# Kernel optimization log

Measured on AMD Instinct MI355X. Metric: run time of the kernel, lower is better.

Reference implementation:

```python
import jax, jax.numpy as jnp
import numpy as np
import math

B, L, D, H = 2, 2048, 1024, 16
HD = D // H          # head_dim = 64
DF = 4096            # d_feedforward
SIGMA = 0.02


def setup_inputs() -> dict:
    key = jax.random.key(0)
    ks = jax.random.split(key, 18)
    g = lambda k, shape: (jax.random.normal(k, shape, jnp.float32) * SIGMA)
    inp = {
        "x": jax.random.normal(ks[0], (B, L, D), jnp.float32),
        # causal mask: True above diagonal -> masked
        "causal_mask": jnp.triu(jnp.ones((L, L), dtype=bool), 1),
        # attention weights, stored [in, out] (math-equivalent to torch Linear)
        "Wq": g(ks[1], (D, D)), "bq": jnp.zeros((D,), jnp.float32),
        "Wk": g(ks[2], (D, D)), "bk": jnp.zeros((D,), jnp.float32),
        "Wv": g(ks[3], (D, D)), "bv": jnp.zeros((D,), jnp.float32),
        "Wo": g(ks[4], (D, D)), "bo": jnp.zeros((D,), jnp.float32),
        "ln1_g": jnp.ones((D,), jnp.float32), "ln1_b": jnp.zeros((D,), jnp.float32),
        "W1": g(ks[5], (D, DF)), "b1": jnp.zeros((DF,), jnp.float32),
        "W2": g(ks[6], (DF, D)), "b2": jnp.zeros((D,), jnp.float32),
        "ln2_g": jnp.ones((D,), jnp.float32), "ln2_b": jnp.zeros((D,), jnp.float32),
    }
    return inp


def _layernorm(x, g, b, eps=1e-5):
    m = jnp.mean(x, axis=-1, keepdims=True)
    v = jnp.mean((x - m) ** 2, axis=-1, keepdims=True)
    return (x - m) * jax.lax.rsqrt(v + eps) * g + b


def _rita_gelu(h):
    return h * 0.5 * (1.0 + jnp.tanh(0.79788456 * h * (1.0 + 0.044715 * h * h)))


def _rotate_half(x):
    x1, x2 = x[..., : x.shape[-1] // 2], x[..., x.shape[-1] // 2 :]
    return jnp.concatenate((-x2, x1), axis=-1)


def _rope_tables(seq_len, head_dim, dtype):
    inv_freq = 1.0 / (10000.0 ** (jnp.arange(0, head_dim, 2, dtype=jnp.float32) / head_dim))
    t = jnp.arange(seq_len, dtype=jnp.float32)
    freqs = jnp.einsum("i,j->ij", t, inv_freq)          # [L, HD/2]
    emb = jnp.concatenate((freqs, freqs), axis=-1)        # [L, HD]
    return jnp.cos(emb).astype(dtype)[None, None], jnp.sin(emb).astype(dtype)[None, None]


def reference(x, causal_mask, Wq, bq, Wk, bk, Wv, bv, Wo, bo,
              ln1_g, ln1_b, W1, b1, W2, b2, ln2_g, ln2_b):
    N, Lx, Dx = x.shape
    # --- attention block ---
    y = _layernorm(x, ln1_g, ln1_b)
    def heads(t):  # [N,L,D] -> [N,H,L,HD]
        return t.reshape(N, Lx, H, HD).transpose(0, 2, 1, 3)
    q = heads(y @ Wq + bq)
    k = heads(y @ Wk + bk)
    v = heads(y @ Wv + bv)
    cos, sin = _rope_tables(Lx, HD, x.dtype)
    q = q * cos + _rotate_half(q) * sin
    k = k * cos + _rotate_half(k) * sin
    att = jnp.einsum("nhqd,nhkd->nhqk", q, k) * (1.0 / math.sqrt(HD))
    att = jnp.where(causal_mask[None, None], jnp.float32(-jnp.inf).astype(att.dtype), att)
    att = jax.nn.softmax(att, axis=-1)
    o = jnp.einsum("nhqk,nhkd->nhqd", att, v)
    o = o.transpose(0, 2, 1, 3).reshape(N, Lx, Dx)
    y = o @ Wo + bo
    x = x + y
    # --- MLP block ---
    y = _layernorm(x, ln2_g, ln2_b)
    y = _rita_gelu(y @ W1 + b1) @ W2 + b2
    return x + y
```

## Files before the change

### kernel.cpp

```cpp
#include <hip/hip_runtime.h>
#include <math.h>

#define B_  2
#define L_  2048
#define D_  1024
#define H_  16
#define HD_ 64
#define DF_ 4096
#define NR_ 4096

typedef __bf16 bf16_t;
typedef bf16_t bf16x8 __attribute__((ext_vector_type(8)));
typedef float  f32x4  __attribute__((ext_vector_type(4)));
typedef unsigned short u16;
typedef u16 u16x8 __attribute__((ext_vector_type(8)));
typedef u16 u16x4 __attribute__((ext_vector_type(4)));
typedef unsigned int u32;
typedef u32 u32x2 __attribute__((ext_vector_type(2)));

__device__ __forceinline__ u16 f2bf(float f) {
  unsigned u = __float_as_uint(f);
  u += 0x7fffu + ((u >> 16) & 1u);
  return (u16)(u >> 16);
}
__device__ __forceinline__ float bf2f(u16 s) {
  return __uint_as_float(((unsigned)s) << 16);
}
__device__ __forceinline__ float gelu_f(float h) {
  return h * 0.5f * (1.f + tanhf(0.79788456f * h * (1.f + 0.044715f * h * h)));
}

__device__ __forceinline__ void async_copy16(void* lds, const void* g) {
  __builtin_amdgcn_global_load_lds(
      (const __attribute__((address_space(1))) unsigned int*)g,
      (__attribute__((address_space(3))) unsigned int*)lds, 16, 0, 0);
}

__global__ __launch_bounds__(256) void transpose_conv(
    const float* __restrict__ W, u16* __restrict__ out, int K, int N) {
  __shared__ float T[64][65];
  const int tid = threadIdx.x;
  const int n0 = blockIdx.x * 64, k0 = blockIdx.y * 64;
  const int r = tid >> 2, c4 = (tid & 3) * 16;
  const float* src = W + (size_t)(k0 + r) * N + n0 + c4;
#pragma unroll
  for (int i = 0; i < 16; i += 4) {
    float4 f = *(const float4*)(src + i);
    T[r][c4 + i + 0] = f.x; T[r][c4 + i + 1] = f.y;
    T[r][c4 + i + 2] = f.z; T[r][c4 + i + 3] = f.w;
  }
  __syncthreads();
  u16* dst = out + (size_t)(n0 + r) * K + k0 + c4;
#pragma unroll
  for (int half = 0; half < 2; ++half) {
    u16x8 o8;
#pragma unroll
    for (int i = 0; i < 8; ++i) o8[i] = f2bf(T[c4 + half * 8 + i][r]);
    *(u16x8*)(dst + half * 8) = o8;
  }
}

__global__ __launch_bounds__(256) void concat_bias(
    const float* __restrict__ bq, const float* __restrict__ bk,
    const float* __restrict__ bv, float* __restrict__ bqkv) {
  int i = blockIdx.x * 256 + threadIdx.x;
  if (i < 3072) {
    float v = (i < 1024) ? bq[i] : (i < 2048) ? bk[i - 1024] : bv[i - 2048];
    bqkv[i] = v;
  }
}

__global__ __launch_bounds__(256) void rope_tables(
    float* __restrict__ cosT, float* __restrict__ sinT) {
  int i = blockIdx.x * 256 + threadIdx.x;
  int pos = i >> 5, d = i & 31;
  float invf = powf(10000.f, -(float)d / 32.f);
  float a = (float)pos * invf;
  cosT[i] = cosf(a);
  sinT[i] = sinf(a);
}

__global__ __launch_bounds__(256) void rope_apply(
    u16* __restrict__ qkv, const float* __restrict__ cosT,
    const float* __restrict__ sinT) {
  int i = blockIdx.x * 256 + threadIdx.x;
  int d0 = (i & 3) * 8;
  int hh = (i >> 2) & 15;
  int qk = (i >> 6) & 1;
  int row = i >> 7;
  int pos = row & (L_ - 1);
  size_t base = (size_t)row * 3072 + qk * 1024 + hh * 64 + d0;
  u16x8 a = *(const u16x8*)(qkv + base);
  u16x8 bb = *(const u16x8*)(qkv + base + 32);
  float4 c0 = *(const float4*)(cosT + pos * 32 + d0);
  float4 c1 = *(const float4*)(cosT + pos * 32 + d0 + 4);
  float4 s0 = *(const float4*)(sinT + pos * 32 + d0);
  float4 s1 = *(const float4*)(sinT + pos * 32 + d0 + 4);
  const float qs = qk ? 1.f : 0.18033688f;
  u16x8 ra, rb;
#pragma unroll
  for (int j = 0; j < 8; ++j) {
    float co = (j < 4) ? ((const float*)&c0)[j] : ((const float*)&c1)[j - 4];
    float si = (j < 4) ? ((const float*)&s0)[j] : ((const float*)&s1)[j - 4];
    float v0 = bf2f(a[j]), v1 = bf2f(bb[j]);
    ra[j] = f2bf((v0 * co - v1 * si) * qs);
    rb[j] = f2bf((v1 * co + v0 * si) * qs);
  }
  *(u16x8*)(qkv + base) = ra;
  *(u16x8*)(qkv + base + 32) = rb;
}

__global__ __launch_bounds__(256) void v_transpose(
    const u16* __restrict__ qkv, u16* __restrict__ vt) {
  const int tid = threadIdx.x;
  const int d = tid & 63, sub = tid >> 6;
  const int s0 = (blockIdx.x * 4 + sub) * 8;
  const int bh = blockIdx.y, b = bh >> 4, h = bh & 15;
  u16x8 o;
#pragma unroll
  for (int i = 0; i < 8; ++i)
    o[i] = qkv[(size_t)(b * L_ + s0 + i) * 3072 + 2048 + h * 64 + d];
  *(u16x8*)(vt + ((size_t)bh * 64 + d) * 2048 + s0) = o;
}

__global__ __launch_bounds__(256) void ln_kernel(
    const float* __restrict__ x, const float* __restrict__ gm,
    const float* __restrict__ bt, u16* __restrict__ out) {
  const int row = blockIdx.x, tid = threadIdx.x;
  const float4 v = ((const float4*)(x + (size_t)row * D_))[tid];
  float s = v.x + v.y + v.z + v.w;
#pragma unroll
  for (int m = 1; m < 64; m <<= 1) s += __shfl_xor(s, m);
  __shared__ float red[4], red2[4];
  if ((tid & 63) == 0) red[tid >> 6] = s;
  __syncthreads();
  const float mean = (red[0] + red[1] + red[2] + red[3]) * (1.f / D_);
  float d0 = v.x - mean, d1 = v.y - mean, d2 = v.z - mean, d3 = v.w - mean;
  float sq = d0 * d0 + d1 * d1 + d2 * d2 + d3 * d3;
#pragma unroll
  for (int m = 1; m < 64; m <<= 1) sq += __shfl_xor(sq, m);
  if ((tid & 63) == 0) red2[tid >> 6] = sq;
  __syncthreads();
  const float var = (red2[0] + red2[1] + red2[2] + red2[3]) * (1.f / D_);
  const float rstd = rsqrtf(var + 1e-5f);
  const int c = tid * 4;
  u16x4 o;
  o[0] = f2bf(d0 * rstd * gm[c + 0] + bt[c + 0]);
  o[1] = f2bf(d1 * rstd * gm[c + 1] + bt[c + 1]);
  o[2] = f2bf(d2 * rstd * gm[c + 2] + bt[c + 2]);
  o[3] = f2bf(d3 * rstd * gm[c + 3] + bt[c + 3]);
  ((u16x4*)(out + (size_t)row * D_))[tid] = o;
}

template <int EPI>
__global__ __launch_bounds__(256) void gemm_bt(
    const u16* __restrict__ A, const u16* __restrict__ Bt,
    const float* __restrict__ bias, const float* __restrict__ resid,
    void* __restrict__ out, int M, int N, int K) {
  __shared__ u16 As[128 * 32];
  __shared__ u16 Bs[128 * 32];
  const int tid = threadIdx.x;
  const int l = tid & 63, wid = tid >> 6;
  const int m0 = blockIdx.y * 128, n0 = blockIdx.x * 128;
  const int wr = wid >> 1, wc = wid & 1;

  f32x4 acc[4][4];
#pragma unroll
  for (int mi = 0; mi < 4; ++mi)
#pragma unroll
    for (int ni = 0; ni < 4; ++ni) acc[mi][ni] = (f32x4){0.f, 0.f, 0.f, 0.f};

  for (int kb = 0; kb < K; kb += 32) {
#pragma unroll
    for (int r = 0; r < 2; ++r) {
      const int fo = r * 4096 + tid * 16;
      const int row = fo >> 6, cb = fo & 63;
      async_copy16((char*)As + fo, A + (size_t)(m0 + row) * K + kb + (cb >> 1));
      async_copy16((char*)Bs + fo, Bt + (size_t)(n0 + row) * K + kb + (cb >> 1));
    }
    __syncthreads();
    bf16x8 ag[4], bg[4];
#pragma unroll
    for (int mi = 0; mi < 4; ++mi) {
      int row = wr * 64 + mi * 16 + (l & 15);
      ag[mi] = *(const bf16x8*)((const char*)As + row * 64 + ((l >> 4) * 16));
    }
#pragma unroll
    for (int ni = 0; ni < 4; ++ni) {
      int row = wc * 64 + ni * 16 + (l & 15);
      bg[ni] = *(const bf16x8*)((const char*)Bs + row * 64 + ((l >> 4) * 16));
    }
#pragma unroll
    for (int mi = 0; mi < 4; ++mi)
#pragma unroll
      for (int ni = 0; ni < 4; ++ni)
        acc[mi][ni] = __builtin_amdgcn_mfma_f32_16x16x32_bf16(
            ag[mi], bg[ni], acc[mi][ni], 0, 0, 0);
    __syncthreads();
  }

  const int cl = l & 15, rq = l >> 4;
#pragma unroll
  for (int ni = 0; ni < 4; ++ni) {
    const int col = n0 + wc * 64 + ni * 16 + cl;
    const float bv = bias[col];
#pragma unroll
    for (int mi = 0; mi < 4; ++mi) {
#pragma unroll
      for (int j = 0; j < 4; ++j) {
        const int rowg = m0 + wr * 64 + mi * 16 + rq * 4 + j;
        float v = acc[mi][ni][j] + bv;
        if (EPI == 0) {
          ((u16*)out)[(size_t)rowg * N + col] = f2bf(v);
        } else if (EPI == 1) {
          ((u16*)out)[(size_t)rowg * N + col] = f2bf(gelu_f(v));
        } else {
          ((float*)out)[(size_t)rowg * N + col] =
              v + resid[(size_t)rowg * N + col];
        }
      }
    }
  }
}

__global__ __launch_bounds__(256, 4) void attn_kernel(
    const u16* __restrict__ qkv, const u16* __restrict__ vt,
    u16* __restrict__ o) {
  const int tid = threadIdx.x, l = tid & 63, wid = tid >> 6;
  const int id = blockIdx.x;
  const int seq = id >> 3, xcd = id & 7;
  const int bh = xcd * 4 + (seq & 3);
  const int qblk = 31 - (seq >> 2);
  const int b = bh >> 4, h = bh & 15;
  const int q0 = qblk * 64;

  __shared__ u16 Ks[2][64 * 64];
  __shared__ u16 Vs[2][64 * 64];
  __shared__ u16 Ps[4][16 * 64];

  const int r16 = l & 15, g = l >> 4;

  const int srow = tid >> 3, scb = (tid & 7) * 16;
  const int scol = (scb ^ ((srow & 7) << 4)) >> 1;
  const u16* ksrc = qkv + (size_t)(b * L_ + srow) * 3072 + 1024 + h * 64 + scol;
  const u16* vsrc = vt + ((size_t)bh * 64 + srow) * 2048 + scol;

#define STAGE_KV(BUF, KB) do {                                              \
    async_copy16((char*)&Ks[BUF][0] + tid * 16,                             \
                 ksrc + (size_t)(KB) * 3072);                               \
    async_copy16((char*)&Ks[BUF][0] + tid * 16 + 4096,                      \
                 ksrc + (size_t)(KB) * 3072 + 32 * 3072);                   \
    async_copy16((char*)&Vs[BUF][0] + tid * 16, vsrc + (KB));               \
    async_copy16((char*)&Vs[BUF][0] + tid * 16 + 4096,                      \
                 vsrc + (KB) + 32 * 2048);                                  \
  } while (0)

  const int qrow_g = b * L_ + q0 + wid * 16 + r16;
  const u16* qp = qkv + (size_t)qrow_g * 3072 + h * 64 + g * 8;
  const bf16x8 qb0 = *(const bf16x8*)qp;
  const bf16x8 qb1 = *(const bf16x8*)(qp + 32);

  float m_ = -1e30f, ls = 0.f;
  f32x4 oa[4];
#pragma unroll
  for (int t = 0; t < 4; ++t) oa[t] = (f32x4){0.f, 0.f, 0.f, 0.f};

  char* const psw = (char*)&Ps[wid][0] + r16 * 128;
  const int pswz = (r16 & 7) << 4;

  const int nt = qblk + 1;
  int buf = 0;
  STAGE_KV(0, 0);

  for (int it = 0; it < nt; ++it) {
    const int kb = it * 64;
    const bool diag = (it == nt - 1);
    STAGE_KV(buf ^ 1, diag ? kb : kb + 64);
    asm volatile("s_waitcnt vmcnt(4)" ::: "memory");
    __builtin_amdgcn_s_barrier();

    const char* kb_l = (const char*)&Ks[0][0] + buf * 8192;
    const char* vb_l = (const char*)&Vs[0][0] + buf * 8192;

    float p[4][4];
#pragma unroll
    for (int t = 0; t < 4; ++t) {
      if (diag && t > wid) {
#pragma unroll
        for (int j = 0; j < 4; ++j) p[t][j] = -1e30f;
        continue;
      }
      const int krow = t * 16 + r16, swzk = (krow & 7) << 4;
      bf16x8 k0 = *(const bf16x8*)(kb_l + krow * 128 + ((g * 16) ^ swzk));
      bf16x8 k1 = *(const bf16x8*)(kb_l + krow * 128 + ((64 + g * 16) ^ swzk));
      f32x4 s = (f32x4){0.f, 0.f, 0.f, 0.f};
      s = __builtin_amdgcn_mfma_f32_16x16x32_bf16(k0, qb0, s, 0, 0, 0);
      s = __builtin_amdgcn_mfma_f32_16x16x32_bf16(k1, qb1, s, 0, 0, 0);
      if (diag && t == wid) {
#pragma unroll
        for (int j = 0; j < 4; ++j)
          p[t][j] = (g * 4 + j <= r16) ? s[j] : -1e30f;
      } else {
#pragma unroll
        for (int j = 0; j < 4; ++j) p[t][j] = s[j];
      }
    }

    float pm = -1e30f;
#pragma unroll
    for (int t = 0; t < 4; ++t)
#pragma unroll
      for (int j = 0; j < 4; ++j) pm = fmaxf(pm, p[t][j]);
    pm = fmaxf(pm, __shfl_xor(pm, 16));
    pm = fmaxf(pm, __shfl_xor(pm, 32));
    const float mn = fmaxf(m_, pm);
    const float sc = exp2f(m_ - mn);
    float rs = 0.f;
#pragma unroll
    for (int t = 0; t < 4; ++t)
#pragma unroll
      for (int j = 0; j < 4; ++j) { p[t][j] = exp2f(p[t][j] - mn); rs += p[t][j]; }
    rs += __shfl_xor(rs, 16);
    rs += __shfl_xor(rs, 32);
    ls = ls * sc + rs;
    m_ = mn;
#pragma unroll
    for (int t = 0; t < 4; ++t) oa[t] *= sc;

#pragma unroll
    for (int t = 0; t < 4; ++t) {
      u32x2 w;
      w[0] = (u32)f2bf(p[t][0]) | ((u32)f2bf(p[t][1]) << 16);
      w[1] = (u32)f2bf(p[t][2]) | ((u32)f2bf(p[t][3]) << 16);
      *(u32x2*)(psw + ((t * 32 + g * 8) ^ pswz)) = w;
    }

#pragma unroll
    for (int kc = 0; kc < 2; ++kc) {
      bf16x8 pf = *(const bf16x8*)(psw + ((kc * 64 + g * 16) ^ pswz));
#pragma unroll
      for (int t = 0; t < 4; ++t) {
        const int vrow = t * 16 + r16, swzv = (vrow & 7) << 4;
        bf16x8 vf = *(const bf16x8*)(vb_l + vrow * 128 +
                                     ((kc * 64 + g * 16) ^ swzv));
        oa[t] = __builtin_amdgcn_mfma_f32_16x16x32_bf16(vf, pf, oa[t], 0, 0, 0);
      }
    }

    __builtin_amdgcn_s_barrier();
    buf ^= 1;
  }
#undef STAGE_KV

  const float inv = 1.f / ls;
  u16* op = o + (size_t)qrow_g * D_ + h * 64;
#pragma unroll
  for (int t = 0; t < 4; ++t)
#pragma unroll
    for (int j = 0; j < 4; ++j)
      op[t * 16 + g * 4 + j] = f2bf(oa[t][j] * inv);
}

extern "C" void kernel_launch(void* const* d_in, const int* in_sizes, int n_in,
                              void* d_out, int out_size, void* d_ws, size_t ws_size,
                              hipStream_t stream) {
  (void)in_sizes; (void)n_in; (void)out_size; (void)ws_size;
  const float* x    = (const float*)d_in[0];
  const float* Wq   = (const float*)d_in[2];
  const float* bq   = (const float*)d_in[3];
  const float* Wk   = (const float*)d_in[4];
  const float* bk   = (const float*)d_in[5];
  const float* Wv   = (const float*)d_in[6];
  const float* bv   = (const float*)d_in[7];
  const float* Wo   = (const float*)d_in[8];
  const float* bo   = (const float*)d_in[9];
  const float* ln1g = (const float*)d_in[10];
  const float* ln1b = (const float*)d_in[11];
  const float* W1   = (const float*)d_in[12];
  const float* b1   = (const float*)d_in[13];
  const float* W2   = (const float*)d_in[14];
  const float* b2   = (const float*)d_in[15];
  const float* ln2g = (const float*)d_in[16];
  const float* ln2b = (const float*)d_in[17];
  float* out = (float*)d_out;
  char* ws = (char*)d_ws;

  u16*   wqkvT = (u16*)(ws + 0);
  u16*   woT   = (u16*)(ws + 6291456);
  u16*   w1T   = (u16*)(ws + 8388608);
  u16*   w2T   = (u16*)(ws + 16777216);
  float* bqkv  = (float*)(ws + 25165824);
  float* cosT  = (float*)(ws + 25178112);
  float* sinT  = (float*)(ws + 25440256);
  float* x2    = (float*)(ws + 25702400);
  u16*   lnbuf = (u16*)(ws + 42479616);
  u16*   vtb   = lnbuf;
  u16*   qkv   = (u16*)(ws + 50868224);
  u16*   attnO = (u16*)(ws + 76034048);
  u16*   hbuf  = qkv;

  const dim3 blk(256);
  transpose_conv<<<dim3(16, 16), blk, 0, stream>>>(Wq, wqkvT, 1024, 1024);
  transpose_conv<<<dim3(16, 16), blk, 0, stream>>>(Wk, wqkvT + 1024 * 1024, 1024, 1024);
  transpose_conv<<<dim3(16, 16), blk, 0, stream>>>(Wv, wqkvT + 2048 * 1024, 1024, 1024);
  transpose_conv<<<dim3(16, 16), blk, 0, stream>>>(Wo, woT, 1024, 1024);
  transpose_conv<<<dim3(64, 16), blk, 0, stream>>>(W1, w1T, 1024, 4096);
  transpose_conv<<<dim3(16, 64), blk, 0, stream>>>(W2, w2T, 4096, 1024);
  concat_bias<<<12, blk, 0, stream>>>(bq, bk, bv, bqkv);
  rope_tables<<<256, blk, 0, stream>>>(cosT, sinT);

  ln_kernel<<<NR_, blk, 0, stream>>>(x, ln1g, ln1b, lnbuf);
  gemm_bt<0><<<dim3(24, 32), blk, 0, stream>>>(lnbuf, wqkvT, bqkv, nullptr,
                                               qkv, NR_, 3072, 1024);
  rope_apply<<<2048, blk, 0, stream>>>(qkv, cosT, sinT);
  v_transpose<<<dim3(64, 32), blk, 0, stream>>>(qkv, vtb);
  attn_kernel<<<1024, blk, 0, stream>>>(qkv, vtb, attnO);

  gemm_bt<2><<<dim3(8, 32), blk, 0, stream>>>(attnO, woT, bo, x, x2,
                                              NR_, 1024, 1024);
  ln_kernel<<<NR_, blk, 0, stream>>>(x2, ln2g, ln2b, lnbuf);
  gemm_bt<1><<<dim3(32, 32), blk, 0, stream>>>(lnbuf, w1T, b1, nullptr,
                                               hbuf, NR_, 4096, 1024);
  gemm_bt<2><<<dim3(8, 32), blk, 0, stream>>>(hbuf, w2T, b2, x2, out,
                                              NR_, 1024, 4096);
}
```

Measured before the change: 455.1 us.

## Double-buffer GEMM shared tiles and remap blocks for XCD/L2 locality

The GEMM kernel now uses two LDS buffers and issues the async global loads for the next K-slice before computing on the current one. It waits with a vmcnt count so load latency overlaps the MFMA work. It also moves to a 1D grid with a block-id swizzle that spreads consecutive ids across the 8 XCDs and groups 8 row-tiles per column strip, aiming for better L2 reuse. The cost is double the LDS use, which can reduce occupancy, and the raw barrier and waitcnt scheme relies on the async copies retiring in order.

```diff
diff --git a/kernel.cpp b/kernel.cpp
--- a/kernel.cpp
+++ b/kernel.cpp
@@ -156,13 +156,34 @@
 __global__ __launch_bounds__(256) void gemm_bt(
     const u16* __restrict__ A, const u16* __restrict__ Bt,
     const float* __restrict__ bias, const float* __restrict__ resid,
-    void* __restrict__ out, int M, int N, int K) {
-  __shared__ u16 As[128 * 32];
-  __shared__ u16 Bs[128 * 32];
+    void* __restrict__ out, int M, int N, int K, int gx) {
+  __shared__ u16 As[2][128 * 32];
+  __shared__ u16 Bs[2][128 * 32];
   const int tid = threadIdx.x;
   const int l = tid & 63, wid = tid >> 6;
-  const int m0 = blockIdx.y * 128, n0 = blockIdx.x * 128;
+  const int nwg = (int)gridDim.x, cpx = nwg >> 3;
+  const int id = (int)blockIdx.x;
+  const int wgid = (id & 7) * cpx + (id >> 3);
+  const int strip = wgid / (8 * gx);
+  const int rr = wgid - strip * 8 * gx;
+  const int m0 = (strip * 8 + (rr & 7)) * 128;
+  const int n0 = (rr >> 3) * 128;
   const int wr = wid >> 1, wc = wid & 1;
+  const int r16 = l & 15, g = l >> 4;
+
+  const int fo0 = tid * 16;
+  const int row0 = fo0 >> 6, ce0 = (fo0 & 63) >> 1;
+  const u16* a_lo = A + (size_t)(m0 + row0) * K + ce0;
+  const u16* a_hi = A + (size_t)(m0 + 64 + row0) * K + ce0;
+  const u16* b_lo = Bt + (size_t)(n0 + row0) * K + ce0;
+  const u16* b_hi = Bt + (size_t)(n0 + 64 + row0) * K + ce0;
+
+#define STAGE_G(BUF, KB) do {                                   \
+    async_copy16((char*)&As[BUF][0] + fo0, a_lo + (KB));        \
+    async_copy16((char*)&As[BUF][0] + fo0 + 4096, a_hi + (KB)); \
+    async_copy16((char*)&Bs[BUF][0] + fo0, b_lo + (KB));        \
+    async_copy16((char*)&Bs[BUF][0] + fo0 + 4096, b_hi + (KB)); \
+  } while (0)
 
   f32x4 acc[4][4];
 #pragma unroll
@@ -170,36 +191,37 @@
 #pragma unroll
     for (int ni = 0; ni < 4; ++ni) acc[mi][ni] = (f32x4){0.f, 0.f, 0.f, 0.f};
 
-  for (int kb = 0; kb < K; kb += 32) {
-#pragma unroll
-    for (int r = 0; r < 2; ++r) {
-      const int fo = r * 4096 + tid * 16;
-      const int row = fo >> 6, cb = fo & 63;
-      async_copy16((char*)As + fo, A + (size_t)(m0 + row) * K + kb + (cb >> 1));
-      async_copy16((char*)Bs + fo, Bt + (size_t)(n0 + row) * K + kb + (cb >> 1));
-    }
-    __syncthreads();
+  const int nk = K >> 5;
+  int buf = 0;
+  STAGE_G(0, 0);
+  for (int it = 0; it < nk; ++it) {
+    const int nxt = ((it + 1 < nk) ? it + 1 : it) << 5;
+    STAGE_G(buf ^ 1, nxt);
+    asm volatile("s_waitcnt vmcnt(4)" ::: "memory");
+    __builtin_amdgcn_s_barrier();
+
+    const char* ab = (const char*)&As[buf][0];
+    const char* bb = (const char*)&Bs[buf][0];
     bf16x8 ag[4], bg[4];
 #pragma unroll
-    for (int mi = 0; mi < 4; ++mi) {
-      int row = wr * 64 + mi * 16 + (l & 15);
-      ag[mi] = *(const bf16x8*)((const char*)As + row * 64 + ((l >> 4) * 16));
-    }
-#pragma unroll
-    for (int ni = 0; ni < 4; ++ni) {
-      int row = wc * 64 + ni * 16 + (l & 15);
-      bg[ni] = *(const bf16x8*)((const char*)Bs + row * 64 + ((l >> 4) * 16));
-    }
+    for (int mi = 0; mi < 4; ++mi)
+      ag[mi] = *(const bf16x8*)(ab + (wr * 64 + mi * 16 + r16) * 64 + g * 16);
+#pragma unroll
+    for (int ni = 0; ni < 4; ++ni)
+      bg[ni] = *(const bf16x8*)(bb + (wc * 64 + ni * 16 + r16) * 64 + g * 16);
 #pragma unroll
     for (int mi = 0; mi < 4; ++mi)
 #pragma unroll
       for (int ni = 0; ni < 4; ++ni)
         acc[mi][ni] = __builtin_amdgcn_mfma_f32_16x16x32_bf16(
             ag[mi], bg[ni], acc[mi][ni], 0, 0, 0);
-    __syncthreads();
-  }
-
-  const int cl = l & 15, rq = l >> 4;
+
+    __builtin_amdgcn_s_barrier();
+    buf ^= 1;
+  }
+#undef STAGE_G
+
+  const int cl = r16, rq = g;
 #pragma unroll
   for (int ni = 0; ni < 4; ++ni) {
     const int col = n0 + wc * 64 + ni * 16 + cl;
@@ -410,17 +432,17 @@
   rope_tables<<<256, blk, 0, stream>>>(cosT, sinT);
 
   ln_kernel<<<NR_, blk, 0, stream>>>(x, ln1g, ln1b, lnbuf);
-  gemm_bt<0><<<dim3(24, 32), blk, 0, stream>>>(lnbuf, wqkvT, bqkv, nullptr,
-                                               qkv, NR_, 3072, 1024);
+  gemm_bt<0><<<768, blk, 0, stream>>>(lnbuf, wqkvT, bqkv, nullptr,
+                                      qkv, NR_, 3072, 1024, 24);
   rope_apply<<<2048, blk, 0, stream>>>(qkv, cosT, sinT);
   v_transpose<<<dim3(64, 32), blk, 0, stream>>>(qkv, vtb);
   attn_kernel<<<1024, blk, 0, stream>>>(qkv, vtb, attnO);
 
-  gemm_bt<2><<<dim3(8, 32), blk, 0, stream>>>(attnO, woT, bo, x, x2,
-                                              NR_, 1024, 1024);
+  gemm_bt<2><<<256, blk, 0, stream>>>(attnO, woT, bo, x, x2,
+                                      NR_, 1024, 1024, 8);
   ln_kernel<<<NR_, blk, 0, stream>>>(x2, ln2g, ln2b, lnbuf);
-  gemm_bt<1><<<dim3(32, 32), blk, 0, stream>>>(lnbuf, w1T, b1, nullptr,
-                                               hbuf, NR_, 4096, 1024);
-  gemm_bt<2><<<dim3(8, 32), blk, 0, stream>>>(hbuf, w2T, b2, x2, out,
-                                              NR_, 1024, 4096);
-}
+  gemm_bt<1><<<1024, blk, 0, stream>>>(lnbuf, w1T, b1, nullptr,
+                                       hbuf, NR_, 4096, 1024, 32);
+  gemm_bt<2><<<256, blk, 0, stream>>>(hbuf, w2T, b2, x2, out,
+                                      NR_, 1024, 4096, 8);
+}
```

Result: no change. 450.2 us (-1.1%).
